# Kernel tuning notes

Hardware: AMD Instinct MI355X
Metric: run time of the kernel (lower is better)

## Reference

```python
import jax, jax.numpy as jnp
import numpy as np

GAMMA = 1.0


def setup_inputs() -> dict:
    key = jax.random.key(0)
    kx, ky = jax.random.split(key)
    x = jax.random.normal(kx, (8192, 128), dtype=jnp.float32)
    y = jax.random.normal(ky, (8192, 128), dtype=jnp.float32)
    return {"x": x, "y": y}


def reference(x, y):
    # RBF kernel K[i,j] = exp(-gamma * ||x_i - y_j||^2)
    x2 = jnp.sum(x * x, axis=1)              # [N]
    y2 = jnp.sum(y * y, axis=1)              # [M]
    xy = jnp.einsum('nd,md->nm', x, y)       # [N, M] GEMM
    sq = x2[:, None] + y2[None, :] - 2.0 * xy
    sq = jnp.maximum(sq, 0.0)                # guard tiny negatives from cancellation
    return jnp.exp(-GAMMA * sq)
```

## Files before the change

### kernel.cpp

```cpp
#include <hip/hip_runtime.h>
#include <hip/hip_bf16.h>

typedef __bf16 bf16x8 __attribute__((ext_vector_type(8)));
typedef float f32x4 __attribute__((ext_vector_type(4)));
typedef float f32x16 __attribute__((ext_vector_type(16)));
typedef unsigned short us4 __attribute__((ext_vector_type(4)));

#define NLOG2E  -1.44269504088896340736f
#define TWOLOG2E 2.88539008177792681472f

__device__ __forceinline__ unsigned short f2bf(float f) {
    unsigned u = __float_as_uint(f);
    u += 0x7fffu + ((u >> 16) & 1u);
    return (unsigned short)(u >> 16);
}

__global__ __launch_bounds__(256)
void rbf_prep(const float* __restrict__ X, const float* __restrict__ Y,
              unsigned short* __restrict__ Xb, unsigned short* __restrict__ Yb,
              float* __restrict__ x2n, float* __restrict__ y2n) {
    const int b = blockIdx.x;
    const float* src = (b < 256) ? X : Y;
    unsigned short* db = (b < 256) ? Xb : Yb;
    float* dn = (b < 256) ? x2n : y2n;
    const int r0 = (b & 255) * 32;
    const int t = threadIdx.x;

    const f32x4* s4 = (const f32x4*)(src + (size_t)r0 * 128);
#pragma unroll
    for (int i = 0; i < 4; ++i) {
        int idx = i * 256 + t;
        int r = idx >> 5, c4 = idx & 31;
        f32x4 v = s4[idx];
        us4 o;
        o.x = f2bf(v[0]); o.y = f2bf(v[1]); o.z = f2bf(v[2]); o.w = f2bf(v[3]);
        int pc = (c4 >> 1) ^ (r & 7);
        *(us4*)&db[(size_t)(r0 + r) * 128 + pc * 8 + (c4 & 1) * 4] = o;
    }

    {
        int r = t >> 3, sub = t & 7;
        const f32x4* row = (const f32x4*)(src + (size_t)(r0 + r) * 128);
        float s = 0.f;
#pragma unroll
        for (int c = 0; c < 4; ++c) {
            f32x4 v = row[sub * 4 + c];
            s += v[0] * v[0] + v[1] * v[1] + v[2] * v[2] + v[3] * v[3];
        }
        s += __shfl_xor(s, 1);
        s += __shfl_xor(s, 2);
        s += __shfl_xor(s, 4);
        if (sub == 0) dn[r0 + r] = NLOG2E * s;
    }
}

__global__ __launch_bounds__(256, 3)
void rbf_main(const unsigned short* __restrict__ Xb, const unsigned short* __restrict__ Yb,
              const float* __restrict__ x2n, const float* __restrict__ y2n,
              float* __restrict__ O, int ldo) {
    __shared__ __align__(16) char smem[49152];

    const int t = threadIdx.x, l = t & 63, w = t >> 6;
    const int col0 = blockIdx.x * 128, row0 = blockIdx.y * 64;

    const char* gA = (const char*)(Xb + (size_t)row0 * 128);
    const char* gB = (const char*)(Yb + (size_t)col0 * 128);
#pragma unroll
    for (int j = 0; j < 4; ++j) {
        int base = (w * 4 + j) * 1024;
        __builtin_amdgcn_global_load_lds(
            (const __attribute__((address_space(1))) void*)(gA + base + l * 16),
            (__attribute__((address_space(3))) void*)(smem + base), 16, 0, 0);
    }
#pragma unroll
    for (int j = 0; j < 8; ++j) {
        int base = (w * 8 + j) * 1024;
        __builtin_amdgcn_global_load_lds(
            (const __attribute__((address_space(1))) void*)(gB + base + l * 16),
            (__attribute__((address_space(3))) void*)(smem + 16384 + base), 16, 0, 0);
    }

    const int ln = l & 31, hi = l >> 5;
    const int wr = (w >> 1) * 32, wcw = (w & 1) * 64;

    f32x4 xv[4];
#pragma unroll
    for (int g = 0; g < 4; ++g)
        xv[g] = *(const f32x4*)&x2n[row0 + wr + 8 * g + 4 * hi];
    float ynp[2];
#pragma unroll
    for (int nf = 0; nf < 2; ++nf)
        ynp[nf] = y2n[col0 + wcw + nf * 32 + ln];

    __syncthreads();

    f32x16 acc0 = {}, acc1 = {};
    const int RA = wr + ln;
    const int C0 = wcw + ln;
    const int C1 = wcw + 32 + ln;
#pragma unroll
    for (int kk = 0; kk < 8; ++kk) {
        int lc = 2 * kk + hi;
        bf16x8 af = *(const bf16x8*)(smem + RA * 256 + ((lc ^ (RA & 7)) * 16));
        bf16x8 b0 = *(const bf16x8*)(smem + 16384 + C0 * 256 + ((lc ^ (C0 & 7)) * 16));
        bf16x8 b1 = *(const bf16x8*)(smem + 16384 + C1 * 256 + ((lc ^ (C1 & 7)) * 16));
        acc0 = __builtin_amdgcn_mfma_f32_32x32x16_bf16(af, b0, acc0, 0, 0, 0);
        acc1 = __builtin_amdgcn_mfma_f32_32x32x16_bf16(af, b1, acc1, 0, 0, 0);
    }

#pragma unroll
    for (int nf = 0; nf < 2; ++nf) {
        float yb = ynp[nf];
        float* ob = &O[(size_t)(row0 + wr + 4 * hi) * ldo + col0 + wcw + nf * 32 + ln];
#pragma unroll
        for (int g = 0; g < 4; ++g) {
#pragma unroll
            for (int i = 0; i < 4; ++i) {
                float xy = (nf == 0) ? acc0[g * 4 + i] : acc1[g * 4 + i];
                float arg = fmaf(TWOLOG2E, xy, xv[g][i] + yb);
                arg = fminf(arg, 0.f);
                __builtin_nontemporal_store(exp2f(arg), &ob[(size_t)(8 * g + i) * ldo]);
            }
        }
    }
}

extern "C" void kernel_launch(void* const* d_in, const int* in_sizes, int n_in,
                              void* d_out, int out_size, void* d_ws, size_t ws_size,
                              hipStream_t stream) {
    const float* X = (const float*)d_in[0];
    const float* Y = (const float*)d_in[1];
    float* O = (float*)d_out;
    const int N = in_sizes[0] / 128;
    const int M = in_sizes[1] / 128;
    unsigned short* Xb = (unsigned short*)d_ws;
    unsigned short* Yb = Xb + (size_t)N * 128;
    float* x2n = (float*)(Yb + (size_t)M * 128);
    float* y2n = x2n + N;
    rbf_prep<<<dim3((N + M) / 32), 256, 0, stream>>>(X, Y, Xb, Yb, x2n, y2n);
    rbf_main<<<dim3(M / 128, N / 64), 256, 0, stream>>>(Xb, Yb, x2n, y2n, O, M);
}
```

Before: 266.9 us.

## Pre-pack bf16 operands into MFMA fragment order and load directly from global

The prep kernel now writes X and Y in bf16, pre-arranged in the exact per-lane fragment layout the 32x32x16 MFMA expects, in 32-row panels. The main kernel then drops the LDS staging, the swizzle and the block barrier, and each lane reads its 16-byte operand fragments straight from global memory or cache. Launch bounds rise to 4 blocks per CU now that no shared memory is used. The trade-off is that operands shared by waves in a block are fetched from L1/L2 once per wave instead of once per block, which adds cache traffic and exposes global-load latency directly in the MFMA loop.

```diff
diff --git a/kernel.cpp b/kernel.cpp
--- a/kernel.cpp
+++ b/kernel.cpp
@@ -4,7 +4,7 @@
 typedef __bf16 bf16x8 __attribute__((ext_vector_type(8)));
 typedef float f32x4 __attribute__((ext_vector_type(4)));
 typedef float f32x16 __attribute__((ext_vector_type(16)));
-typedef unsigned short us4 __attribute__((ext_vector_type(4)));
+typedef unsigned short us8 __attribute__((ext_vector_type(8)));
 
 #define NLOG2E  -1.44269504088896340736f
 #define TWOLOG2E 2.88539008177792681472f
@@ -17,29 +17,33 @@
 
 __global__ __launch_bounds__(256)
 void rbf_prep(const float* __restrict__ X, const float* __restrict__ Y,
-              unsigned short* __restrict__ Xb, unsigned short* __restrict__ Yb,
+              char* __restrict__ Xp, char* __restrict__ Yp,
               float* __restrict__ x2n, float* __restrict__ y2n) {
     const int b = blockIdx.x;
     const float* src = (b < 256) ? X : Y;
-    unsigned short* db = (b < 256) ? Xb : Yb;
+    char* db = (b < 256) ? Xp : Yp;
     float* dn = (b < 256) ? x2n : y2n;
-    const int r0 = (b & 255) * 32;
+    const int p = b & 255;
+    const int r0 = p * 32;
     const int t = threadIdx.x;
 
-    const f32x4* s4 = (const f32x4*)(src + (size_t)r0 * 128);
-#pragma unroll
-    for (int i = 0; i < 4; ++i) {
-        int idx = i * 256 + t;
-        int r = idx >> 5, c4 = idx & 31;
-        f32x4 v = s4[idx];
-        us4 o;
-        o.x = f2bf(v[0]); o.y = f2bf(v[1]); o.z = f2bf(v[2]); o.w = f2bf(v[3]);
-        int pc = (c4 >> 1) ^ (r & 7);
-        *(us4*)&db[(size_t)(r0 + r) * 128 + pc * 8 + (c4 & 1) * 4] = o;
+    {
+        const int ln = t & 31, s = t >> 5;
+        const f32x4* row = (const f32x4*)(src + (size_t)(r0 + ln) * 128);
+        f32x4 v0 = row[s * 4 + 0], v1 = row[s * 4 + 1];
+        f32x4 v2 = row[s * 4 + 2], v3 = row[s * 4 + 3];
+        us8 lo, hh;
+        lo[0] = f2bf(v0[0]); lo[1] = f2bf(v0[1]); lo[2] = f2bf(v0[2]); lo[3] = f2bf(v0[3]);
+        lo[4] = f2bf(v1[0]); lo[5] = f2bf(v1[1]); lo[6] = f2bf(v1[2]); lo[7] = f2bf(v1[3]);
+        hh[0] = f2bf(v2[0]); hh[1] = f2bf(v2[1]); hh[2] = f2bf(v2[2]); hh[3] = f2bf(v2[3]);
+        hh[4] = f2bf(v3[0]); hh[5] = f2bf(v3[1]); hh[6] = f2bf(v3[2]); hh[7] = f2bf(v3[3]);
+        char* dst = db + (size_t)p * 8192 + s * 1024 + ln * 16;
+        *(us8*)dst = lo;
+        *(us8*)(dst + 512) = hh;
     }
 
     {
-        int r = t >> 3, sub = t & 7;
+        const int r = t >> 3, sub = t & 7;
         const f32x4* row = (const f32x4*)(src + (size_t)(r0 + r) * 128);
         float s = 0.f;
 #pragma unroll
@@ -54,56 +58,33 @@
     }
 }
 
-__global__ __launch_bounds__(256, 3)
-void rbf_main(const unsigned short* __restrict__ Xb, const unsigned short* __restrict__ Yb,
+__global__ __launch_bounds__(256, 4)
+void rbf_main(const char* __restrict__ Xp, const char* __restrict__ Yp,
               const float* __restrict__ x2n, const float* __restrict__ y2n,
               float* __restrict__ O, int ldo) {
-    __shared__ __align__(16) char smem[49152];
-
     const int t = threadIdx.x, l = t & 63, w = t >> 6;
     const int col0 = blockIdx.x * 128, row0 = blockIdx.y * 64;
+    const int wr = (w >> 1) * 32, wcw = (w & 1) * 64;
+    const int ln = l & 31, hi = l >> 5;
 
-    const char* gA = (const char*)(Xb + (size_t)row0 * 128);
-    const char* gB = (const char*)(Yb + (size_t)col0 * 128);
-#pragma unroll
-    for (int j = 0; j < 4; ++j) {
-        int base = (w * 4 + j) * 1024;
-        __builtin_amdgcn_global_load_lds(
-            (const __attribute__((address_space(1))) void*)(gA + base + l * 16),
-            (__attribute__((address_space(3))) void*)(smem + base), 16, 0, 0);
-    }
-#pragma unroll
-    for (int j = 0; j < 8; ++j) {
-        int base = (w * 8 + j) * 1024;
-        __builtin_amdgcn_global_load_lds(
-            (const __attribute__((address_space(1))) void*)(gB + base + l * 16),
-            (__attribute__((address_space(3))) void*)(smem + 16384 + base), 16, 0, 0);
-    }
-
-    const int ln = l & 31, hi = l >> 5;
-    const int wr = (w >> 1) * 32, wcw = (w & 1) * 64;
+    const char* pa  = Xp + (size_t)((row0 + wr) >> 5) * 8192 + l * 16;
+    const char* pb0 = Yp + (size_t)((col0 + wcw) >> 5) * 8192 + l * 16;
+    const char* pb1 = pb0 + 8192;
 
     f32x4 xv[4];
 #pragma unroll
     for (int g = 0; g < 4; ++g)
         xv[g] = *(const f32x4*)&x2n[row0 + wr + 8 * g + 4 * hi];
     float ynp[2];
-#pragma unroll
-    for (int nf = 0; nf < 2; ++nf)
-        ynp[nf] = y2n[col0 + wcw + nf * 32 + ln];
-
-    __syncthreads();
+    ynp[0] = y2n[col0 + wcw + ln];
+    ynp[1] = y2n[col0 + wcw + 32 + ln];
 
     f32x16 acc0 = {}, acc1 = {};
-    const int RA = wr + ln;
-    const int C0 = wcw + ln;
-    const int C1 = wcw + 32 + ln;
 #pragma unroll
     for (int kk = 0; kk < 8; ++kk) {
-        int lc = 2 * kk + hi;
-        bf16x8 af = *(const bf16x8*)(smem + RA * 256 + ((lc ^ (RA & 7)) * 16));
-        bf16x8 b0 = *(const bf16x8*)(smem + 16384 + C0 * 256 + ((lc ^ (C0 & 7)) * 16));
-        bf16x8 b1 = *(const bf16x8*)(smem + 16384 + C1 * 256 + ((lc ^ (C1 & 7)) * 16));
+        bf16x8 af = *(const bf16x8*)(pa  + kk * 1024);
+        bf16x8 b0 = *(const bf16x8*)(pb0 + kk * 1024);
+        bf16x8 b1 = *(const bf16x8*)(pb1 + kk * 1024);
         acc0 = __builtin_amdgcn_mfma_f32_32x32x16_bf16(af, b0, acc0, 0, 0, 0);
         acc1 = __builtin_amdgcn_mfma_f32_32x32x16_bf16(af, b1, acc1, 0, 0, 0);
     }
@@ -133,10 +114,10 @@
     float* O = (float*)d_out;
     const int N = in_sizes[0] / 128;
     const int M = in_sizes[1] / 128;
-    unsigned short* Xb = (unsigned short*)d_ws;
-    unsigned short* Yb = Xb + (size_t)N * 128;
-    float* x2n = (float*)(Yb + (size_t)M * 128);
+    char* Xp = (char*)d_ws;
+    char* Yp = Xp + (size_t)N * 256;
+    float* x2n = (float*)(Yp + (size_t)M * 256);
     float* y2n = x2n + N;
-    rbf_prep<<<dim3((N + M) / 32), 256, 0, stream>>>(X, Y, Xb, Yb, x2n, y2n);
-    rbf_main<<<dim3(M / 128, N / 64), 256, 0, stream>>>(Xb, Yb, x2n, y2n, O, M);
+    rbf_prep<<<dim3((N + M) / 32), 256, 0, stream>>>(X, Y, Xp, Yp, x2n, y2n);
+    rbf_main<<<dim3(M / 128, N / 64), 256, 0, stream>>>(Xp, Yp, x2n, y2n, O, M);
 }
```

Measured after the change: 268.2 us. No clear change (+0.5%).
